# Performance work log

Hardware: AMD Instinct MI355X
Metric: run time of the kernel (lower is better)

The kernel has to match this reference:

```python
import jax, jax.numpy as jnp
import numpy as np

B, C, FULLBIN, T = 4, 2, 1025, 1024
BINS = 1024            # n_fft // 2
BANDS = 4
D = BINS // BANDS      # 256
FF = 2048
FF2, FF4 = FF // 2, FF // 4
CROP = 1024
EPS = 1e-5


def layernorm(x, g, b):
    m = jnp.mean(x, axis=-1, keepdims=True)
    v = jnp.mean(jnp.square(x - m), axis=-1, keepdims=True)
    return (x - m) * jax.lax.rsqrt(v + EPS) * g + b


def dconv(x, w, pad):
    # depthwise Conv1d: x (B, Cc, L), w (Cc, 1, K)
    return jax.lax.conv_general_dilated(
        x, w, window_strides=(1,), padding=[(pad, pad)],
        feature_group_count=x.shape[1],
        dimension_numbers=('NCH', 'OIH', 'NCH'))


def pconv(x, w):
    # pointwise Conv1d: x (B, Ci, L), w (Co, Ci, 1)
    return jnp.einsum('bcl,oc->bol', x, w[:, :, 0])


def reference(src, in_w, ln1_g, ln1_b, glu_w, ln2_g, ln2_b,
              c1L_dw, c1L_pw, c1R_dw, c1R_pw, ln3_g, ln3_b,
              c1M_dw, c1M_pw, ln4_g, ln4_b,
              q_w, q_b, qc_w, qc_b, k_w, k_b, v_w, v_b, o_w, o_b, er,
              ln5_g, ln5_b, c2_w, c3_w, out_w):
    s = src[:, :, :BINS]                                 # (B,C,F,T)
    x = jnp.einsum('bcft,c->btf', s, in_w[0])            # in_project + squeeze -> (B,T,BINS)

    # GLU block
    h = layernorm(x, ln1_g, ln1_b)
    g = h @ glu_w.T                                       # (B,T,2*BINS)
    x = x + g[..., :BINS] * jax.nn.sigmoid(g[..., BINS:])

    # conv feed-forward (note: conv1L applied without transpose, as in original)
    h = layernorm(x, ln2_g, ln2_b)
    hL = jax.nn.relu(pconv(dconv(h, c1L_dw, 5), c1L_pw))                          # (B,FF2,BINS)
    hR = jax.nn.relu(pconv(dconv(jnp.swapaxes(h, 1, 2), c1R_dw, 3), c1R_pw))      # (B,FF4,T)
    hR = jnp.swapaxes(hR, 1, 2)                                                   # (B,T,FF4)
    hR = jnp.pad(hR, ((0, 0), (0, 0), (0, BINS - FF4)))
    h = layernorm(hL + hR, ln3_g, ln3_b)                                          # (B,FF2,BINS)
    h = pconv(dconv(jnp.swapaxes(h, 1, 2), c1M_dw, 3), c1M_pw)                    # (B,BINS,FF2)
    x = x + jnp.swapaxes(h, 1, 2)

    # multiband frame attention (q_conv reused for q,k,v as in original)
    h = layernorm(x, ln4_g, ln4_b)

    def qkv(W, bvec):
        y = h @ W.T + bvec
        y = dconv(jnp.swapaxes(y, 1, 2), qc_w, 3) + qc_b[None, :, None]
        return jnp.swapaxes(y, 1, 2).reshape(B, T, BANDS, D)

    q = qkv(q_w, q_b).transpose(0, 2, 1, 3)              # (B,BANDS,T,D)
    k = qkv(k_w, k_b).transpose(0, 2, 3, 1)              # (B,BANDS,D,T)
    v = qkv(v_w, v_b).transpose(0, 2, 1, 3)              # (B,BANDS,T,D)

    p = jnp.pad(q @ er, ((0, 0), (0, 0), (0, 0), (1, 0)))  # (B,BANDS,T,CROP+1)
    p = jnp.swapaxes(p, 2, 3)[:, :, 1:, :]                 # (B,BANDS,CROP,T)
    qk = (q @ k + p) / jnp.sqrt(jnp.float32(BINS))
    a = jax.nn.softmax(qk, axis=-1)
    o = (a @ v).transpose(0, 2, 1, 3).reshape(B, T, BINS) @ o_w.T + o_b
    x = x + o

    # squared-ReLU MLP
    h = layernorm(x, ln5_g, ln5_b)
    h = jnp.square(jax.nn.relu(h @ c2_w.T)) @ c3_w.T
    x = x + h

    # stack back as extra channel, output head, ReLU1, replicate-pad freq row
    t = jnp.swapaxes(x, 1, 2)[:, None]                   # (B,1,BINS,T)
    s2 = jnp.concatenate([s, t], axis=1)                 # (B,C+1,BINS,T)
    y = jnp.einsum('bcft,oc->boft', s2, out_w)           # (B,2,BINS,T)
    y = jnp.clip(y, 0.0, 6.0) / 6.0
    return jnp.concatenate([y, y[:, :, -1:, :]], axis=2)  # (B,2,FULLBIN,T)


def setup_inputs() -> dict:
    key = jax.random.key(0)
    ks = jax.random.split(key, 20)
    n = lambda i, shape, s=0.02: jax.random.normal(ks[i], shape, jnp.float32) * s
    return {
        'src': jax.random.normal(ks[0], (B, C, FULLBIN, T), jnp.float32),
        'in_w': n(1, (1, C)),
        'ln1_g': jnp.ones((BINS,), jnp.float32), 'ln1_b': jnp.zeros((BINS,), jnp.float32),
        'glu_w': n(2, (2 * BINS, BINS)),
        'ln2_g': jnp.ones((BINS,), jnp.float32), 'ln2_b': jnp.zeros((BINS,), jnp.float32),
        'c1L_dw': n(3, (BINS, 1, 11), 0.1), 'c1L_pw': n(4, (FF2, BINS, 1)),
        'c1R_dw': n(5, (BINS, 1, 7), 0.1), 'c1R_pw': n(6, (FF4, BINS, 1)),
        'ln3_g': jnp.ones((FF2,), jnp.float32), 'ln3_b': jnp.zeros((FF2,), jnp.float32),
        'c1M_dw': n(7, (FF2, 1, 7), 0.1), 'c1M_pw': n(8, (BINS, FF2, 1)),
        'ln4_g': jnp.ones((BINS,), jnp.float32), 'ln4_b': jnp.zeros((BINS,), jnp.float32),
        'q_w': n(9, (BINS, BINS)), 'q_b': jnp.zeros((BINS,), jnp.float32),
        'qc_w': n(10, (BINS, 1, 7), 0.1), 'qc_b': jnp.zeros((BINS,), jnp.float32),
        'k_w': n(11, (BINS, BINS)), 'k_b': jnp.zeros((BINS,), jnp.float32),
        'v_w': n(12, (BINS, BINS)), 'v_b': jnp.zeros((BINS,), jnp.float32),
        'o_w': n(13, (BINS, BINS)), 'o_b': jnp.zeros((BINS,), jnp.float32),
        'er': jax.random.normal(ks[14], (D, CROP), jnp.float32),
        'ln5_g': jnp.ones((BINS,), jnp.float32), 'ln5_b': jnp.zeros((BINS,), jnp.float32),
        'c2_w': n(15, (FF, BINS)), 'c3_w': n(16, (BINS, FF)),
        'out_w': n(17, (2, C + 1)),
    }
```

## Files before the change

### kernel.cpp

```cpp
#include <hip/hip_runtime.h>
#include <math.h>


typedef unsigned short u16;
typedef __attribute__((ext_vector_type(4))) float floatx4;
typedef __attribute__((ext_vector_type(8))) short short8;

#define NB 4
static const long long M1 = 1024LL * 1024LL;

__device__ __forceinline__ float bf2f(u16 h) {
    union { unsigned int u; float f; } v;
    v.u = ((unsigned int)h) << 16;
    return v.f;
}
__device__ __forceinline__ u16 f2bf(float x) {
    union { float f; unsigned int u; } v;
    v.f = x;
    unsigned int r = (v.u + 0x7FFFu + ((v.u >> 16) & 1u)) >> 16;
    return (u16)r;
}

__device__ __forceinline__ void async_cp16(const u16* g, u16* lds) {
    __builtin_amdgcn_global_load_lds(
        (const __attribute__((address_space(1))) unsigned int*)g,
        (__attribute__((address_space(3))) unsigned int*)lds, 16, 0, 0);
}

__device__ __forceinline__ float block_sum(float v) {
    __shared__ float sd[4];
    #pragma unroll
    for (int off = 32; off; off >>= 1) v += __shfl_down(v, off, 64);
    int lane = threadIdx.x & 63, wid = threadIdx.x >> 6;
    __syncthreads();
    if (lane == 0) sd[wid] = v;
    __syncthreads();
    return sd[0] + sd[1] + sd[2] + sd[3];
}


template<int BM, int BN, int ACT, bool ACCUM, bool OBF>
__global__ __launch_bounds__(256)
void gemm_bf(const u16* __restrict__ A, const u16* __restrict__ B,
             void* __restrict__ Cv, int K, int lda, int ldb, int ldc,
             long long sAz, long long sBz, long long sCz,
             const float* __restrict__ bias, float scale)
{
    constexpr int MI = BM / 32;
    constexpr int NJ = BN / 32;

    A += (long long)blockIdx.z * sAz;
    B += (long long)blockIdx.z * sBz;
    const long long zc = (long long)blockIdx.z * sCz;

    __shared__ u16 As[BM * 64];
    __shared__ u16 Bs[BN * 64];

    const int id = blockIdx.x + gridDim.x * blockIdx.y;
    const int bx = (id >> 3) % gridDim.x;
    const int by = (id & 7) + 8 * ((id >> 3) / gridDim.x);
    const int m0 = by * BM;
    const int n0 = bx * BN;

    const int lane = threadIdx.x & 63;
    const int w    = threadIdx.x >> 6;
    const int wm   = (w >> 1) * (BM / 2);
    const int wn   = (w & 1) * (BN / 2);
    const int srow = lane >> 2;
    const int scol = (lane & 3) * 8;

    floatx4 acc[MI][NJ];
    #pragma unroll
    for (int i = 0; i < MI; i++)
        #pragma unroll
        for (int j = 0; j < NJ; j++)
            acc[i][j] = floatx4{0.f, 0.f, 0.f, 0.f};

    for (int k0 = 0; k0 < K; k0 += 64) {
        #pragma unroll
        for (int r = 0; r < BM / 32; r++) {
            const int inst = w * (BM / 32) + r;
            const int rg = inst >> 1, kb = inst & 1;
            async_cp16(A + (long long)(m0 + rg * 16 + srow) * lda + k0 + kb * 32 + scol,
                       &As[(rg * 2 + kb) * 512]);
        }
        #pragma unroll
        for (int r = 0; r < BN / 32; r++) {
            const int inst = w * (BN / 32) + r;
            const int rg = inst >> 1, kb = inst & 1;
            async_cp16(B + (long long)(n0 + rg * 16 + srow) * ldb + k0 + kb * 32 + scol,
                       &Bs[(rg * 2 + kb) * 512]);
        }
        __syncthreads();

        #pragma unroll
        for (int s = 0; s < 2; s++) {
            short8 a[MI], b[NJ];
            const int fr = lane & 15;
            const int q  = lane >> 4;
            const int go = (fr * 4 + q) * 8;
            #pragma unroll
            for (int i = 0; i < MI; i++)
                a[i] = *(const short8*)&As[(((wm >> 4) + i) * 2 + s) * 512 + go];
            #pragma unroll
            for (int j = 0; j < NJ; j++)
                b[j] = *(const short8*)&Bs[(((wn >> 4) + j) * 2 + s) * 512 + go];
            #pragma unroll
            for (int i = 0; i < MI; i++)
                #pragma unroll
                for (int j = 0; j < NJ; j++)
                    acc[i][j] = __builtin_amdgcn_mfma_f32_16x16x32_bf16(
                        a[i], b[j], acc[i][j], 0, 0, 0);
        }
        __syncthreads();
    }

    float* Cf = (float*)Cv;
    u16*  Cb  = (u16*)Cv;
    const int cn    = n0 + wn + (lane & 15);
    const int rbase = m0 + wm + (lane >> 4) * 4;
    float bj[NJ];
    #pragma unroll
    for (int j = 0; j < NJ; j++) bj[j] = bias ? bias[cn + j * 16] : 0.f;

    #pragma unroll
    for (int i = 0; i < MI; i++) {
        #pragma unroll
        for (int r = 0; r < 4; r++) {
            const int m = rbase + i * 16 + r;
            #pragma unroll
            for (int j = 0; j < NJ; j++) {
                const int n = cn + j * 16;
                float v = (acc[i][j][r] + bj[j]) * scale;
                if (ACT == 1) v = fmaxf(v, 0.f);
                else if (ACT == 2) { v = fmaxf(v, 0.f); v = v * v; }
                const long long ci = zc + (long long)m * ldc + n;
                if (OBF)        Cb[ci] = f2bf(v);
                else if (ACCUM) Cf[ci] += v;
                else            Cf[ci] = v;
            }
        }
    }
}

__global__ __launch_bounds__(256)
void glugemm_k(const u16* __restrict__ A, const u16* __restrict__ B1,
               const u16* __restrict__ B2, float* __restrict__ X)
{
    constexpr int BM = 128, BN = 64, MI = 4, NJ = 2;
    __shared__ u16 As[BM * 64];
    __shared__ u16 B1s[BN * 64];
    __shared__ u16 B2s[BN * 64];

    const int id = blockIdx.x + gridDim.x * blockIdx.y;
    const int bx = (id >> 3) % gridDim.x;
    const int by = (id & 7) + 8 * ((id >> 3) / gridDim.x);
    const int m0 = by * BM;
    const int n0 = bx * BN;

    const int lane = threadIdx.x & 63;
    const int w    = threadIdx.x >> 6;
    const int wm   = (w >> 1) * 64;
    const int wn   = (w & 1) * 32;
    const int srow = lane >> 2;
    const int scol = (lane & 3) * 8;

    floatx4 acc1[MI][NJ], acc2[MI][NJ];
    #pragma unroll
    for (int i = 0; i < MI; i++)
        #pragma unroll
        for (int j = 0; j < NJ; j++) {
            acc1[i][j] = floatx4{0.f, 0.f, 0.f, 0.f};
            acc2[i][j] = floatx4{0.f, 0.f, 0.f, 0.f};
        }

    for (int k0 = 0; k0 < 1024; k0 += 64) {
        #pragma unroll
        for (int r = 0; r < 4; r++) {
            const int inst = w * 4 + r;
            const int rg = inst >> 1, kb = inst & 1;
            async_cp16(A + (long long)(m0 + rg * 16 + srow) * 1024 + k0 + kb * 32 + scol,
                       &As[(rg * 2 + kb) * 512]);
        }
        #pragma unroll
        for (int r = 0; r < 2; r++) {
            const int inst = w * 2 + r;
            const int rg = inst >> 1, kb = inst & 1;
            async_cp16(B1 + (long long)(n0 + rg * 16 + srow) * 1024 + k0 + kb * 32 + scol,
                       &B1s[(rg * 2 + kb) * 512]);
            async_cp16(B2 + (long long)(n0 + rg * 16 + srow) * 1024 + k0 + kb * 32 + scol,
                       &B2s[(rg * 2 + kb) * 512]);
        }
        __syncthreads();

        #pragma unroll
        for (int s = 0; s < 2; s++) {
            short8 a[MI], b1[NJ], b2[NJ];
            const int fr = lane & 15;
            const int q  = lane >> 4;
            const int go = (fr * 4 + q) * 8;
            #pragma unroll
            for (int i = 0; i < MI; i++)
                a[i] = *(const short8*)&As[(((wm >> 4) + i) * 2 + s) * 512 + go];
            #pragma unroll
            for (int j = 0; j < NJ; j++) {
                b1[j] = *(const short8*)&B1s[(((wn >> 4) + j) * 2 + s) * 512 + go];
                b2[j] = *(const short8*)&B2s[(((wn >> 4) + j) * 2 + s) * 512 + go];
            }
            #pragma unroll
            for (int i = 0; i < MI; i++)
                #pragma unroll
                for (int j = 0; j < NJ; j++) {
                    acc1[i][j] = __builtin_amdgcn_mfma_f32_16x16x32_bf16(
                        a[i], b1[j], acc1[i][j], 0, 0, 0);
                    acc2[i][j] = __builtin_amdgcn_mfma_f32_16x16x32_bf16(
                        a[i], b2[j], acc2[i][j], 0, 0, 0);
                }
        }
        __syncthreads();
    }

    const int cn    = n0 + wn + (lane & 15);
    const int rbase = m0 + wm + (lane >> 4) * 4;
    #pragma unroll
    for (int i = 0; i < MI; i++)
        #pragma unroll
        for (int r = 0; r < 4; r++) {
            const int m = rbase + i * 16 + r;
            #pragma unroll
            for (int j = 0; j < NJ; j++) {
                const int n = cn + j * 16;
                float g = acc1[i][j][r] / (1.f + expf(-acc2[i][j][r]));
                X[(long long)m * 1024 + n] += g;
            }
        }
}

__global__ __launch_bounds__(256)
void sgemm_exp_k(const u16* __restrict__ A, const u16* __restrict__ B,
                 u16* __restrict__ S, float* __restrict__ rowsum, float scale)
{
    constexpr int BM = 128, BN = 128, MI = 4, NJ = 4;
    A += (long long)blockIdx.z * 524288;
    B += (long long)blockIdx.z * 524288;
    S += (long long)blockIdx.z * M1;
    rowsum += blockIdx.z << 10;

    __shared__ u16 As[BM * 64];
    __shared__ u16 Bs[BN * 64];

    const int id = blockIdx.x + gridDim.x * blockIdx.y;
    const int bx = (id >> 3) % gridDim.x;
    const int by = (id & 7) + 8 * ((id >> 3) / gridDim.x);
    const int m0 = by * BM;
    const int n0 = bx * BN;

    const int lane = threadIdx.x & 63;
    const int w    = threadIdx.x >> 6;
    const int wm   = (w >> 1) * 64;
    const int wn   = (w & 1) * 64;
    const int srow = lane >> 2;
    const int scol = (lane & 3) * 8;

    floatx4 acc[MI][NJ];
    #pragma unroll
    for (int i = 0; i < MI; i++)
        #pragma unroll
        for (int j = 0; j < NJ; j++)
            acc[i][j] = floatx4{0.f, 0.f, 0.f, 0.f};

    for (int k0 = 0; k0 < 512; k0 += 64) {
        #pragma unroll
        for (int r = 0; r < 4; r++) {
            const int inst = w * 4 + r;
            const int rg = inst >> 1, kb = inst & 1;
            async_cp16(A + (long long)(m0 + rg * 16 + srow) * 512 + k0 + kb * 32 + scol,
                       &As[(rg * 2 + kb) * 512]);
            async_cp16(B + (long long)(n0 + rg * 16 + srow) * 512 + k0 + kb * 32 + scol,
                       &Bs[(rg * 2 + kb) * 512]);
        }
        __syncthreads();
        #pragma unroll
        for (int s = 0; s < 2; s++) {
            short8 a[MI], b[NJ];
            const int fr = lane & 15;
            const int q  = lane >> 4;
            const int go = (fr * 4 + q) * 8;
            #pragma unroll
            for (int i = 0; i < MI; i++)
                a[i] = *(const short8*)&As[(((wm >> 4) + i) * 2 + s) * 512 + go];
            #pragma unroll
            for (int j = 0; j < NJ; j++)
                b[j] = *(const short8*)&Bs[(((wn >> 4) + j) * 2 + s) * 512 + go];
            #pragma unroll
            for (int i = 0; i < MI; i++)
                #pragma unroll
                for (int j = 0; j < NJ; j++)
                    acc[i][j] = __builtin_amdgcn_mfma_f32_16x16x32_bf16(
                        a[i], b[j], acc[i][j], 0, 0, 0);
        }
        __syncthreads();
    }

    const int cn    = n0 + wn + (lane & 15);
    const int rbase = m0 + wm + (lane >> 4) * 4;
    #pragma unroll
    for (int i = 0; i < MI; i++)
        #pragma unroll
        for (int r = 0; r < 4; r++) {
            const int m = rbase + i * 16 + r;
            float part = 0.f;
            #pragma unroll
            for (int j = 0; j < NJ; j++) {
                const int n = cn + j * 16;
                float e = expf(acc[i][j][r] * scale);
                S[(long long)m * 1024 + n] = f2bf(e);
                part += e;
            }
            #pragma unroll
            for (int off = 8; off; off >>= 1) part += __shfl_xor(part, off, 64);
            if ((lane & 15) == 0) atomicAdd(&rowsum[m], part);
        }
}

__global__ __launch_bounds__(256)
void aogemm_k(const u16* __restrict__ Sb, const u16* __restrict__ Vt,
              const float* __restrict__ rowsum, u16* __restrict__ AO)
{
    constexpr int BM = 128, BN = 64, MI = 4, NJ = 2;
    const int z = blockIdx.z;
    Sb += (long long)z * M1;
    Vt += (long long)z * 262144;
    rowsum += z << 10;
    const long long zc = (long long)(z >> 2) * M1 + (z & 3) * 256;

    __shared__ u16 As[BM * 64];
    __shared__ u16 Bs[BN * 64];

    const int id = blockIdx.x + gridDim.x * blockIdx.y;
    const int bx = (id >> 3) % gridDim.x;
    const int by = (id & 7) + 8 * ((id >> 3) / gridDim.x);
    const int m0 = by * BM;
    const int n0 = bx * BN;

    const int lane = threadIdx.x & 63;
    const int w    = threadIdx.x >> 6;
    const int wm   = (w >> 1) * 64;
    const int wn   = (w & 1) * 32;
    const int srow = lane >> 2;
    const int scol = (lane & 3) * 8;

    floatx4 acc[MI][NJ];
    #pragma unroll
    for (int i = 0; i < MI; i++)
        #pragma unroll
        for (int j = 0; j < NJ; j++)
            acc[i][j] = floatx4{0.f, 0.f, 0.f, 0.f};

    for (int k0 = 0; k0 < 1024; k0 += 64) {
        #pragma unroll
        for (int r = 0; r < 4; r++) {
            const int inst = w * 4 + r;
            const int rg = inst >> 1, kb = inst & 1;
            async_cp16(Sb + (long long)(m0 + rg * 16 + srow) * 1024 + k0 + kb * 32 + scol,
                       &As[(rg * 2 + kb) * 512]);
        }
        #pragma unroll
        for (int r = 0; r < 2; r++) {
            const int inst = w * 2 + r;
            const int rg = inst >> 1, kb = inst & 1;
            async_cp16(Vt + (long long)(n0 + rg * 16 + srow) * 1024 + k0 + kb * 32 + scol,
                       &Bs[(rg * 2 + kb) * 512]);
        }
        __syncthreads();
        #pragma unroll
        for (int s = 0; s < 2; s++) {
            short8 a[MI], b[NJ];
            const int fr = lane & 15;
            const int q  = lane >> 4;
            const int go = (fr * 4 + q) * 8;
            #pragma unroll
            for (int i = 0; i < MI; i++)
                a[i] = *(const short8*)&As[(((wm >> 4) + i) * 2 + s) * 512 + go];
            #pragma unroll
            for (int j = 0; j < NJ; j++)
                b[j] = *(const short8*)&Bs[(((wn >> 4) + j) * 2 + s) * 512 + go];
            #pragma unroll
            for (int i = 0; i < MI; i++)
                #pragma unroll
                for (int j = 0; j < NJ; j++)
                    acc[i][j] = __builtin_amdgcn_mfma_f32_16x16x32_bf16(
                        a[i], b[j], acc[i][j], 0, 0, 0);
        }
        __syncthreads();
    }

    const int cn    = n0 + wn + (lane & 15);
    const int rbase = m0 + wm + (lane >> 4) * 4;
    #pragma unroll
    for (int i = 0; i < MI; i++)
        #pragma unroll
        for (int r = 0; r < 4; r++) {
            const int m = rbase + i * 16 + r;
            const float inv = 1.f / rowsum[m];
            #pragma unroll
            for (int j = 0; j < NJ; j++) {
                const int n = cn + j * 16;
                AO[zc + (long long)m * 1024 + n] = f2bf(acc[i][j][r] * inv);
            }
        }
}

__global__ __launch_bounds__(256)
void ln_bf_k(const float* __restrict__ in, u16* __restrict__ out,
             const float* __restrict__ g, const float* __restrict__ b)
{
    long long row = blockIdx.x;
    const float4* ip = (const float4*)(in + (row << 10));
    int tid = threadIdx.x;
    float4 v = ip[tid];
    float s = v.x + v.y + v.z + v.w;
    s = block_sum(s);
    float mean = s * (1.f / 1024.f);
    float dx = v.x - mean, dy = v.y - mean, dz = v.z - mean, dw = v.w - mean;
    float s2 = dx * dx + dy * dy + dz * dz + dw * dw;
    s2 = block_sum(s2);
    float inv = rsqrtf(s2 * (1.f / 1024.f) + 1e-5f);
    float4 gg = ((const float4*)g)[tid];
    float4 bb = ((const float4*)b)[tid];
    ushort4 o;
    o.x = f2bf(dx * inv * gg.x + bb.x);
    o.y = f2bf(dy * inv * gg.y + bb.y);
    o.z = f2bf(dz * inv * gg.z + bb.z);
    o.w = f2bf(dw * inv * gg.w + bb.w);
    ((ushort4*)(out + (row << 10)))[tid] = o;
}

__global__ __launch_bounds__(256)
void inproj_k(const float* __restrict__ src, const float* __restrict__ inw,
              float* __restrict__ X)
{
    __shared__ float tile[32][33];
    int b = blockIdx.z;
    int f0 = blockIdx.y * 32, t0 = blockIdx.x * 32;
    float w0 = inw[0], w1 = inw[1];
    for (int r = threadIdx.y; r < 32; r += 8) {
        int f = f0 + r, t = t0 + threadIdx.x;
        float s0 = src[(((long long)b * 2 + 0) * 1025 + f) * 1024 + t];
        float s1 = src[(((long long)b * 2 + 1) * 1025 + f) * 1024 + t];
        tile[r][threadIdx.x] = w0 * s0 + w1 * s1;
    }
    __syncthreads();
    for (int r = threadIdx.y; r < 32; r += 8)
        X[((long long)b * 1024 + t0 + r) * 1024 + f0 + threadIdx.x] = tile[threadIdx.x][r];
}

__global__ __launch_bounds__(256)
void dconvF_t_k(const u16* __restrict__ in, u16* __restrict__ out,
                const float* __restrict__ w)
{
    __shared__ float itile[32][44];
    __shared__ float otile[32][33];
    int b = blockIdx.z, t0 = blockIdx.y * 32, f0 = blockIdx.x * 32;
    int tx = threadIdx.x & 31, ty = threadIdx.x >> 5;
    for (int r = ty; r < 32; r += 8)
        for (int c = tx; c < 42; c += 32) {
            int f = f0 - 5 + c;
            itile[r][c] = (f >= 0 && f < 1024)
                ? bf2f(in[((long long)(b * 1024 + t0 + r)) * 1024 + f]) : 0.f;
        }
    __syncthreads();
    for (int r = ty; r < 32; r += 8) {
        const float* wr = w + (t0 + r) * 11;
        float acc = 0.f;
        #pragma unroll
        for (int k = 0; k < 11; k++) acc += itile[r][tx + k] * wr[k];
        otile[tx][r] = acc;
    }
    __syncthreads();
    for (int r = ty; r < 32; r += 8)
        out[((long long)(b * 1024 + f0 + r)) * 1024 + t0 + tx] = f2bf(otile[r][tx]);
}

__global__ __launch_bounds__(256)
void dconvT_bf_k(const u16* __restrict__ in, u16* __restrict__ out,
                 const float* __restrict__ w)
{
    int idx = blockIdx.x * 256 + threadIdx.x;
    int f = idx & 1023;
    int bt = idx >> 10;
    int t = bt & 1023;
    int b = bt >> 10;
    const float* wr = w + f * 7;
    float acc = 0.f;
    #pragma unroll
    for (int k = 0; k < 7; k++) {
        int tt = t + k - 3;
        if (tt >= 0 && tt < 1024)
            acc += bf2f(in[(((long long)b << 10) + tt) * 1024 + f]) * wr[k];
    }
    out[idx] = f2bf(acc);
}

__global__ __launch_bounds__(256)
void vconv_t_k(const u16* __restrict__ T3, u16* __restrict__ out,
               const float* __restrict__ w, const float* __restrict__ bias)
{
    __shared__ float itile[38][32];
    __shared__ float otile[32][33];
    int b = blockIdx.z, t0 = blockIdx.y * 32, f0 = blockIdx.x * 32;
    int tx = threadIdx.x & 31, ty = threadIdx.x >> 5;
    for (int i = threadIdx.x; i < 38 * 32; i += 256) {
        int r = i >> 5, c = i & 31;
        int t = t0 - 3 + r;
        itile[r][c] = (t >= 0 && t < 1024)
            ? bf2f(T3[((long long)(b * 1024 + t)) * 3072 + 2048 + f0 + c]) : 0.f;
    }
    __syncthreads();
    for (int r = ty; r < 32; r += 8) {
        const float* wr = w + (f0 + tx) * 7;
        float acc = bias[f0 + tx];
        #pragma unroll
        for (int k = 0; k < 7; k++) acc += itile[r + k][tx] * wr[k];
        otile[tx][r] = acc;
    }
    __syncthreads();
    for (int r = ty; r < 32; r += 8)
        out[((long long)(b * 1024 + f0 + r)) * 1024 + t0 + tx] = f2bf(otile[r][tx]);
}

__global__ __launch_bounds__(256)
void qkpack_k(const u16* __restrict__ T3, const float* __restrict__ w,
              const float* __restrict__ bias, const u16* __restrict__ ertb,
              u16* __restrict__ Apk, u16* __restrict__ Bpk)
{
    int idx = blockIdx.x * 256 + threadIdx.x;
    int f = idx & 1023;
    int t = (idx >> 10) & 1023;
    int b = idx >> 20;
    int band = f >> 8, d = f & 255, z = (b << 2) | band;
    const float* wr = w + f * 7;
    float bq = bias[f];
    float aq = bq, ak = bq;
    #pragma unroll
    for (int k = 0; k < 7; k++) {
        int tt = t + k - 3;
        if (tt >= 0 && tt < 1024) {
            const u16* row = T3 + ((long long)(b << 10) + tt) * 3072 + f;
            float wk = wr[k];
            aq += bf2f(row[0]) * wk;
            ak += bf2f(row[1024]) * wk;
        }
    }
    long long base = (long long)z * 524288 + t * 512 + d;
    u16 qb = f2bf(aq);
    Apk[base] = qb;
    Apk[base + 256] = ertb[t * 256 + d];
    Bpk[base] = f2bf(ak);
    Bpk[base + 256] = qb;
}

struct CastArgs {
    const float* s[10];
    const float* er; const float* qb; const float* kb; const float* vb;
    u16* ert; float* qkvb;
};
__global__ __launch_bounds__(256)
void castall_k(CastArgs a, u16* __restrict__ dst)
{
    const int sz[10] = {2097152, 1048576, 524288, 1048576, 1048576,
                        1048576, 1048576, 1048576, 2097152, 2097152};
    int seg = blockIdx.y;
    int tid = blockIdx.x * 256 + threadIdx.x;
    if (seg < 10) {
        int n = sz[seg];
        int base = 0;
        for (int i = 0; i < seg; i++) base += sz[i];
        int i4 = tid * 4;
        if (i4 >= n) return;
        float4 v = *(const float4*)(a.s[seg] + i4);
        ushort4 o;
        o.x = f2bf(v.x); o.y = f2bf(v.y); o.z = f2bf(v.z); o.w = f2bf(v.w);
        *(ushort4*)(dst + base + i4) = o;
    } else if (seg == 10) {
        if (tid < 262144) {
            int j = tid >> 8, d = tid & 255;
            a.ert[tid] = f2bf(a.er[d * 1024 + j]);
        }
    } else {
        if (tid < 1024) a.qkvb[tid] = a.qb[tid];
        else if (tid < 2048) a.qkvb[tid] = a.kb[tid - 1024];
        else if (tid < 3072) a.qkvb[tid] = a.vb[tid - 2048];
    }
}

__global__ __launch_bounds__(256)
void out_k(const float* __restrict__ src, const float* __restrict__ X,
           const float* __restrict__ ow, float* __restrict__ out)
{
    __shared__ float tile[32][33];
    int b = blockIdx.z;
    int f0 = blockIdx.y * 32, t0 = blockIdx.x * 32;
    for (int r = threadIdx.y; r < 32; r += 8)
        tile[r][threadIdx.x] = X[((long long)b * 1024 + t0 + r) * 1024 + f0 + threadIdx.x];
    __syncthreads();
    float w00 = ow[0], w01 = ow[1], w02 = ow[2];
    float w10 = ow[3], w11 = ow[4], w12 = ow[5];
    for (int r = threadIdx.y; r < 32; r += 8) {
        int f = f0 + r, t = t0 + threadIdx.x;
        float s0 = src[(((long long)b * 2 + 0) * 1025 + f) * 1024 + t];
        float s1 = src[(((long long)b * 2 + 1) * 1025 + f) * 1024 + t];
        float xv = tile[threadIdx.x][r];
        float v0 = fminf(fmaxf(w00 * s0 + w01 * s1 + w02 * xv, 0.f), 6.f) * (1.f / 6.f);
        float v1 = fminf(fmaxf(w10 * s0 + w11 * s1 + w12 * xv, 0.f), 6.f) * (1.f / 6.f);
        out[(((long long)b * 2 + 0) * 1025 + f) * 1024 + t] = v0;
        out[(((long long)b * 2 + 1) * 1025 + f) * 1024 + t] = v1;
        if (f == 1023) {
            out[(((long long)b * 2 + 0) * 1025 + 1024) * 1024 + t] = v0;
            out[(((long long)b * 2 + 1) * 1025 + 1024) * 1024 + t] = v1;
        }
    }
}

extern "C" void kernel_launch(void* const* d_in, const int* in_sizes, int n_in,
                              void* d_out, int out_size, void* d_ws, size_t ws_size,
                              hipStream_t stream)
{
    const float* src    = (const float*)d_in[0];
    const float* in_w   = (const float*)d_in[1];
    const float* ln1_g  = (const float*)d_in[2];
    const float* ln1_b  = (const float*)d_in[3];
    const float* glu_w  = (const float*)d_in[4];
    const float* ln2_g  = (const float*)d_in[5];
    const float* ln2_b  = (const float*)d_in[6];
    const float* c1L_dw = (const float*)d_in[7];
    const float* c1L_pw = (const float*)d_in[8];
    const float* c1R_dw = (const float*)d_in[9];
    const float* c1R_pw = (const float*)d_in[10];
    const float* ln3_g  = (const float*)d_in[11];
    const float* ln3_b  = (const float*)d_in[12];
    const float* c1M_dw = (const float*)d_in[13];
    const float* c1M_pw = (const float*)d_in[14];
    const float* ln4_g  = (const float*)d_in[15];
    const float* ln4_b  = (const float*)d_in[16];
    const float* q_w    = (const float*)d_in[17];
    const float* q_b    = (const float*)d_in[18];
    const float* qc_w   = (const float*)d_in[19];
    const float* qc_b   = (const float*)d_in[20];
    const float* k_w    = (const float*)d_in[21];
    const float* k_b    = (const float*)d_in[22];
    const float* v_w    = (const float*)d_in[23];
    const float* v_b    = (const float*)d_in[24];
    const float* o_w    = (const float*)d_in[25];
    const float* o_b    = (const float*)d_in[26];
    const float* er     = (const float*)d_in[27];
    const float* ln5_g  = (const float*)d_in[28];
    const float* ln5_b  = (const float*)d_in[29];
    const float* c2_w   = (const float*)d_in[30];
    const float* c3_w   = (const float*)d_in[31];
    const float* out_w  = (const float*)d_in[32];
    float* out = (float*)d_out;

    const size_t MB = 1ull << 20;
    if (ws_size < 162 * MB) return;
    char* wsb = (char*)d_ws;
    float* X     = (float*)(wsb + 0);
    float* SB    = (float*)(wsb + 16 * MB);
    u16* Apk     = (u16*)(wsb + 32 * MB);
    u16* Bpk     = (u16*)(wsb + 48 * MB);
    u16* Hbf     = (u16*)(wsb + 64 * MB);
    u16* T1bf    = (u16*)(wsb + 72 * MB);
    u16* T3      = (u16*)(wsb + 72 * MB);
    float* rowsum= (float*)(wsb + 72 * MB);
    u16* AO      = (u16*)(wsb + 80 * MB);
    u16* T2bf    = (u16*)(wsb + 96 * MB);
    u16* Vt      = (u16*)(wsb + 96 * MB);
    u16* Sbf     = (u16*)(wsb + 104 * MB);
    u16* Gbf     = (u16*)(wsb + 104 * MB);
    u16* W0      = (u16*)(wsb + 136 * MB);

    u16* glu_wb  = W0;
    u16* c1L_pwb = W0 + 2097152;
    u16* c1R_pwb = W0 + 3145728;
    u16* c1M_pwb = W0 + 3670016;
    u16* qkv_wb  = W0 + 4718592;
    u16* o_wb    = W0 + 7864320;
    u16* c2_wb   = W0 + 8912896;
    u16* c3_wb   = W0 + 11010048;
    u16* ertb    = W0 + 13107200;
    float* qkvb  = (float*)(W0 + 13369344);

    const dim3 blk256(256);
    const dim3 tgrid(32, 32, NB);
    const dim3 tblk(32, 8);
    const int EW = 16384;

    CastArgs ca;
    ca.s[0] = glu_w;  ca.s[1] = c1L_pw; ca.s[2] = c1R_pw; ca.s[3] = c1M_pw;
    ca.s[4] = q_w;    ca.s[5] = k_w;    ca.s[6] = v_w;    ca.s[7] = o_w;
    ca.s[8] = c2_w;   ca.s[9] = c3_w;
    ca.er = er; ca.qb = q_b; ca.kb = k_b; ca.vb = v_b;
    ca.ert = ertb; ca.qkvb = qkvb;
    castall_k<<<dim3(2048, 12), blk256, 0, stream>>>(ca, W0);

    inproj_k<<<tgrid, tblk, 0, stream>>>(src, in_w, X);
    ln_bf_k<<<4096, blk256, 0, stream>>>(X, Hbf, ln1_g, ln1_b);
    glugemm_k<<<dim3(16, 32, 1), blk256, 0, stream>>>(
        Hbf, glu_wb, glu_wb + 1048576, X);
    ln_bf_k<<<4096, blk256, 0, stream>>>(X, Hbf, ln2_g, ln2_b);
    dconvF_t_k<<<tgrid, blk256, 0, stream>>>(Hbf, T2bf, c1L_dw);
    gemm_bf<128, 64, 1, false, false><<<dim3(16, 8, NB), blk256, 0, stream>>>(
        c1L_pwb, T2bf, SB, 1024, 1024, 1024, 1024, 0, M1, M1, nullptr, 1.f);
    dconvT_bf_k<<<EW, blk256, 0, stream>>>(Hbf, T1bf, c1R_dw);
    gemm_bf<128, 64, 1, true, false><<<dim3(8, 32, 1), blk256, 0, stream>>>(
        T1bf, c1R_pwb, SB, 1024, 1024, 1024, 1024, 0, 0, 0, nullptr, 1.f);
    ln_bf_k<<<4096, blk256, 0, stream>>>(SB, Hbf, ln3_g, ln3_b);
    dconvT_bf_k<<<EW, blk256, 0, stream>>>(Hbf, T1bf, c1M_dw);
    gemm_bf<128, 64, 0, true, false><<<dim3(16, 32, 1), blk256, 0, stream>>>(
        T1bf, c1M_pwb, X, 1024, 1024, 1024, 1024, 0, 0, 0, nullptr, 1.f);
    ln_bf_k<<<4096, blk256, 0, stream>>>(X, Hbf, ln4_g, ln4_b);
    gemm_bf<128, 128, 0, false, true><<<dim3(24, 32, 1), blk256, 0, stream>>>(
        Hbf, qkv_wb, T3, 1024, 1024, 1024, 3072, 0, 0, 0, qkvb, 1.f);
    qkpack_k<<<EW, blk256, 0, stream>>>(T3, qc_w, qc_b, ertb, Apk, Bpk);
    vconv_t_k<<<tgrid, blk256, 0, stream>>>(T3, Vt, qc_w, qc_b);
    hipMemsetAsync(rowsum, 0, 16 * 1024 * sizeof(float), stream);
    sgemm_exp_k<<<dim3(8, 8, 16), blk256, 0, stream>>>(
        Apk, Bpk, Sbf, rowsum, 0.03125f);
    aogemm_k<<<dim3(4, 8, 16), blk256, 0, stream>>>(Sbf, Vt, rowsum, AO);
    gemm_bf<128, 64, 0, true, false><<<dim3(16, 32, 1), blk256, 0, stream>>>(
        AO, o_wb, X, 1024, 1024, 1024, 1024, 0, 0, 0, o_b, 1.f);
    ln_bf_k<<<4096, blk256, 0, stream>>>(X, Hbf, ln5_g, ln5_b);
    gemm_bf<128, 128, 2, false, true><<<dim3(16, 32, 1), blk256, 0, stream>>>(
        Hbf, c2_wb, Gbf, 1024, 1024, 1024, 2048, 0, 0, 0, nullptr, 1.f);
    gemm_bf<128, 64, 0, true, false><<<dim3(16, 32, 1), blk256, 0, stream>>>(
        Gbf, c3_wb, X, 2048, 2048, 2048, 1024, 0, 0, 0, nullptr, 1.f);
    out_k<<<tgrid, tblk, 0, stream>>>(src, X, out_w, out);
}
```

Before: 602.8 us.

## Store residual stream and SB intermediate in bf16; flatten attention grid mapping

```diff
diff --git a/kernel.cpp b/kernel.cpp
--- a/kernel.cpp
+++ b/kernel.cpp
@@ -38,8 +38,7 @@
     return sd[0] + sd[1] + sd[2] + sd[3];
 }
 
-
-template<int BM, int BN, int ACT, bool ACCUM, bool OBF>
+template<int BM, int BN, int ACT, int OUT>
 __global__ __launch_bounds__(256)
 void gemm_bf(const u16* __restrict__ A, const u16* __restrict__ B,
              void* __restrict__ Cv, int K, int lda, int ldb, int ldc,
@@ -135,9 +134,10 @@
                 if (ACT == 1) v = fmaxf(v, 0.f);
                 else if (ACT == 2) { v = fmaxf(v, 0.f); v = v * v; }
                 const long long ci = zc + (long long)m * ldc + n;
-                if (OBF)        Cb[ci] = f2bf(v);
-                else if (ACCUM) Cf[ci] += v;
-                else            Cf[ci] = v;
+                if (OUT == 0)      Cf[ci] = v;
+                else if (OUT == 1) Cf[ci] += v;
+                else if (OUT == 2) Cb[ci] = f2bf(v);
+                else               Cb[ci] = f2bf(bf2f(Cb[ci]) + v);
             }
         }
     }
@@ -145,7 +145,7 @@
 
 __global__ __launch_bounds__(256)
 void glugemm_k(const u16* __restrict__ A, const u16* __restrict__ B1,
-               const u16* __restrict__ B2, float* __restrict__ X)
+               const u16* __restrict__ B2, u16* __restrict__ X)
 {
     constexpr int BM = 128, BN = 64, MI = 4, NJ = 2;
     __shared__ u16 As[BM * 64];
@@ -231,7 +231,8 @@
             for (int j = 0; j < NJ; j++) {
                 const int n = cn + j * 16;
                 float g = acc1[i][j][r] / (1.f + expf(-acc2[i][j][r]));
-                X[(long long)m * 1024 + n] += g;
+                u16* xp = &X[(long long)m * 1024 + n];
+                *xp = f2bf(bf2f(*xp) + g);
             }
         }
 }
@@ -240,20 +241,24 @@
 void sgemm_exp_k(const u16* __restrict__ A, const u16* __restrict__ B,
                  u16* __restrict__ S, float* __restrict__ rowsum, float scale)
 {
-    constexpr int BM = 128, BN = 128, MI = 4, NJ = 4;
-    A += (long long)blockIdx.z * 524288;
-    B += (long long)blockIdx.z * 524288;
-    S += (long long)blockIdx.z * M1;
-    rowsum += blockIdx.z << 10;
-
-    __shared__ u16 As[BM * 64];
-    __shared__ u16 Bs[BN * 64];
-
-    const int id = blockIdx.x + gridDim.x * blockIdx.y;
-    const int bx = (id >> 3) % gridDim.x;
-    const int by = (id & 7) + 8 * ((id >> 3) / gridDim.x);
-    const int m0 = by * BM;
-    const int n0 = bx * BN;
+    constexpr int MI = 4, NJ = 4;
+    const int i0 = blockIdx.x;
+    const int x  = i0 & 7;
+    const int j0 = i0 >> 3;
+    const int z  = x + 8 * (j0 & 1);
+    const int t  = j0 >> 1;
+    const int bx = t & 7, by = t >> 3;
+
+    A += (long long)z * 524288;
+    B += (long long)z * 524288;
+    S += (long long)z * M1;
+    rowsum += z << 10;
+
+    __shared__ u16 As[128 * 64];
+    __shared__ u16 Bs[128 * 64];
+
+    const int m0 = by * 128;
+    const int n0 = bx * 128;
 
     const int lane = threadIdx.x & 63;
     const int w    = threadIdx.x >> 6;
@@ -327,21 +332,24 @@
 void aogemm_k(const u16* __restrict__ Sb, const u16* __restrict__ Vt,
               const float* __restrict__ rowsum, u16* __restrict__ AO)
 {
-    constexpr int BM = 128, BN = 64, MI = 4, NJ = 2;
-    const int z = blockIdx.z;
+    constexpr int MI = 4, NJ = 2;
+    const int i0 = blockIdx.x;
+    const int x  = i0 & 7;
+    const int j0 = i0 >> 3;
+    const int z  = x + 8 * (j0 & 1);
+    const int t  = j0 >> 1;
+    const int bx = t & 3, by = t >> 2;
+
     Sb += (long long)z * M1;
     Vt += (long long)z * 262144;
     rowsum += z << 10;
     const long long zc = (long long)(z >> 2) * M1 + (z & 3) * 256;
 
-    __shared__ u16 As[BM * 64];
-    __shared__ u16 Bs[BN * 64];
-
-    const int id = blockIdx.x + gridDim.x * blockIdx.y;
-    const int bx = (id >> 3) % gridDim.x;
-    const int by = (id & 7) + 8 * ((id >> 3) / gridDim.x);
-    const int m0 = by * BM;
-    const int n0 = bx * BN;
+    __shared__ u16 As[128 * 64];
+    __shared__ u16 Bs[64 * 64];
+
+    const int m0 = by * 128;
+    const int n0 = bx * 64;
 
     const int lane = threadIdx.x & 63;
     const int w    = threadIdx.x >> 6;
@@ -412,17 +420,17 @@
 }
 
 __global__ __launch_bounds__(256)
-void ln_bf_k(const float* __restrict__ in, u16* __restrict__ out,
+void ln_bf_k(const u16* __restrict__ in, u16* __restrict__ out,
              const float* __restrict__ g, const float* __restrict__ b)
 {
     long long row = blockIdx.x;
-    const float4* ip = (const float4*)(in + (row << 10));
     int tid = threadIdx.x;
-    float4 v = ip[tid];
-    float s = v.x + v.y + v.z + v.w;
+    ushort4 u = ((const ushort4*)(in + (row << 10)))[tid];
+    float x0 = bf2f(u.x), x1 = bf2f(u.y), x2 = bf2f(u.z), x3 = bf2f(u.w);
+    float s = x0 + x1 + x2 + x3;
     s = block_sum(s);
     float mean = s * (1.f / 1024.f);
-    float dx = v.x - mean, dy = v.y - mean, dz = v.z - mean, dw = v.w - mean;
+    float dx = x0 - mean, dy = x1 - mean, dz = x2 - mean, dw = x3 - mean;
     float s2 = dx * dx + dy * dy + dz * dz + dw * dw;
     s2 = block_sum(s2);
     float inv = rsqrtf(s2 * (1.f / 1024.f) + 1e-5f);
@@ -438,7 +446,7 @@
 
 __global__ __launch_bounds__(256)
 void inproj_k(const float* __restrict__ src, const float* __restrict__ inw,
-              float* __restrict__ X)
+              u16* __restrict__ X)
 {
     __shared__ float tile[32][33];
     int b = blockIdx.z;
@@ -452,7 +460,7 @@
     }
     __syncthreads();
     for (int r = threadIdx.y; r < 32; r += 8)
-        X[((long long)b * 1024 + t0 + r) * 1024 + f0 + threadIdx.x] = tile[threadIdx.x][r];
+        X[((long long)b * 1024 + t0 + r) * 1024 + f0 + threadIdx.x] = f2bf(tile[threadIdx.x][r]);
 }
 
 __global__ __launch_bounds__(256)
@@ -595,14 +603,14 @@
 }
 
 __global__ __launch_bounds__(256)
-void out_k(const float* __restrict__ src, const float* __restrict__ X,
+void out_k(const float* __restrict__ src, const u16* __restrict__ X,
            const float* __restrict__ ow, float* __restrict__ out)
 {
     __shared__ float tile[32][33];
     int b = blockIdx.z;
     int f0 = blockIdx.y * 32, t0 = blockIdx.x * 32;
     for (int r = threadIdx.y; r < 32; r += 8)
-        tile[r][threadIdx.x] = X[((long long)b * 1024 + t0 + r) * 1024 + f0 + threadIdx.x];
+        tile[r][threadIdx.x] = bf2f(X[((long long)b * 1024 + t0 + r) * 1024 + f0 + threadIdx.x]);
     __syncthreads();
     float w00 = ow[0], w01 = ow[1], w02 = ow[2];
     float w10 = ow[3], w11 = ow[4], w12 = ow[5];
@@ -664,8 +672,8 @@
     const size_t MB = 1ull << 20;
     if (ws_size < 162 * MB) return;
     char* wsb = (char*)d_ws;
-    float* X     = (float*)(wsb + 0);
-    float* SB    = (float*)(wsb + 16 * MB);
+    u16* X       = (u16*)(wsb + 0);
+    u16* SB      = (u16*)(wsb + 8 * MB);
     u16* Apk     = (u16*)(wsb + 32 * MB);
     u16* Bpk     = (u16*)(wsb + 48 * MB);
     u16* Hbf     = (u16*)(wsb + 64 * MB);
@@ -709,30 +717,29 @@
         Hbf, glu_wb, glu_wb + 1048576, X);
     ln_bf_k<<<4096, blk256, 0, stream>>>(X, Hbf, ln2_g, ln2_b);
     dconvF_t_k<<<tgrid, blk256, 0, stream>>>(Hbf, T2bf, c1L_dw);
-    gemm_bf<128, 64, 1, false, false><<<dim3(16, 8, NB), blk256, 0, stream>>>(
+    gemm_bf<128, 64, 1, 2><<<dim3(16, 8, NB), blk256, 0, stream>>>(
         c1L_pwb, T2bf, SB, 1024, 1024, 1024, 1024, 0, M1, M1, nullptr, 1.f);
     dconvT_bf_k<<<EW, blk256, 0, stream>>>(Hbf, T1bf, c1R_dw);
-    gemm_bf<128, 64, 1, true, false><<<dim3(8, 32, 1), blk256, 0, stream>>>(
+    gemm_bf<128, 64, 1, 3><<<dim3(8, 32, 1), blk256, 0, stream>>>(
         T1bf, c1R_pwb, SB, 1024, 1024, 1024, 1024, 0, 0, 0, nullptr, 1.f);
     ln_bf_k<<<4096, blk256, 0, stream>>>(SB, Hbf, ln3_g, ln3_b);
     dconvT_bf_k<<<EW, blk256, 0, stream>>>(Hbf, T1bf, c1M_dw);
-    gemm_bf<128, 64, 0, true, false><<<dim3(16, 32, 1), blk256, 0, stream>>>(
+    gemm_bf<128, 64, 0, 3><<<dim3(16, 32, 1), blk256, 0, stream>>>(
         T1bf, c1M_pwb, X, 1024, 1024, 1024, 1024, 0, 0, 0, nullptr, 1.f);
     ln_bf_k<<<4096, blk256, 0, stream>>>(X, Hbf, ln4_g, ln4_b);
-    gemm_bf<128, 128, 0, false, true><<<dim3(24, 32, 1), blk256, 0, stream>>>(
+    gemm_bf<128, 128, 0, 2><<<dim3(24, 32, 1), blk256, 0, stream>>>(
         Hbf, qkv_wb, T3, 1024, 1024, 1024, 3072, 0, 0, 0, qkvb, 1.f);
     qkpack_k<<<EW, blk256, 0, stream>>>(T3, qc_w, qc_b, ertb, Apk, Bpk);
     vconv_t_k<<<tgrid, blk256, 0, stream>>>(T3, Vt, qc_w, qc_b);
     hipMemsetAsync(rowsum, 0, 16 * 1024 * sizeof(float), stream);
-    sgemm_exp_k<<<dim3(8, 8, 16), blk256, 0, stream>>>(
-        Apk, Bpk, Sbf, rowsum, 0.03125f);
-    aogemm_k<<<dim3(4, 8, 16), blk256, 0, stream>>>(Sbf, Vt, rowsum, AO);
-    gemm_bf<128, 64, 0, true, false><<<dim3(16, 32, 1), blk256, 0, stream>>>(
+    sgemm_exp_k<<<1024, blk256, 0, stream>>>(Apk, Bpk, Sbf, rowsum, 0.03125f);
+    aogemm_k<<<512, blk256, 0, stream>>>(Sbf, Vt, rowsum, AO);
+    gemm_bf<128, 64, 0, 3><<<dim3(16, 32, 1), blk256, 0, stream>>>(
         AO, o_wb, X, 1024, 1024, 1024, 1024, 0, 0, 0, o_b, 1.f);
     ln_bf_k<<<4096, blk256, 0, stream>>>(X, Hbf, ln5_g, ln5_b);
-    gemm_bf<128, 128, 2, false, true><<<dim3(16, 32, 1), blk256, 0, stream>>>(
+    gemm_bf<128, 128, 2, 2><<<dim3(16, 32, 1), blk256, 0, stream>>>(
         Hbf, c2_wb, Gbf, 1024, 1024, 1024, 2048, 0, 0, 0, nullptr, 1.f);
-    gemm_bf<128, 64, 0, true, false><<<dim3(16, 32, 1), blk256, 0, stream>>>(
+    gemm_bf<128, 64, 0, 3><<<dim3(16, 32, 1), blk256, 0, stream>>>(
         Gbf, c3_wb, X, 2048, 2048, 2048, 1024, 0, 0, 0, nullptr, 1.f);
     out_k<<<tgrid, tblk, 0, stream>>>(src, X, out_w, out);
 }
```

Result: faster. 581.0 us (-3.6%).
